# Kernel tuning notes

Hardware: AMD Instinct MI355X
Metric: run time of the kernel (lower is better)

The kernel has to match this reference:

```python
import jax, jax.numpy as jnp
import numpy as np

N_NODES = 100_000
E_OFF = 1_000_000
HID = 32
GF = 8
NF = 8
N_LAYERS = 3


def _mlp(h, W1, b1, W2, b2):
    # Linear -> ReLU -> Linear (matches MLP([in, hidden, out]))
    return jax.nn.relu(h @ W1 + b1) @ W2 + b2


def _seg_mean(v, idx, n):
    s = jax.ops.segment_sum(v, idx, num_segments=n)
    c = jax.ops.segment_sum(jnp.ones((v.shape[0], 1), v.dtype), idx, num_segments=n)
    return s / jnp.maximum(c, 1.0)


def _graphnet(x, row, col, eattr2, g, p):
    # GraphNet with global block: edge MLP -> mean-aggregate to nodes -> node MLP -> global MLP
    eW1, eb1, eW2, eb2, nW1, nb1, nW2, nb2, gW1, gb1, gW2, gb2 = p
    n, e = x.shape[0], row.shape[0]
    gE = jnp.broadcast_to(g, (e, g.shape[1]))
    e_emb = _mlp(jnp.concatenate([gE, x[row], x[col], eattr2], axis=1), eW1, eb1, eW2, eb2)
    agg = _seg_mean(e_emb, row, n)
    gN = jnp.broadcast_to(g, (n, g.shape[1]))
    n_emb = _mlp(jnp.concatenate([gN, x, agg], axis=1), nW1, nb1, nW2, nb2)
    g_new = _mlp(jnp.concatenate([n_emb.mean(0, keepdims=True), e_emb.mean(0, keepdims=True), g], axis=1),
                 gW1, gb1, gW2, gb2)
    return e_emb, n_emb, g_new


def setup_inputs() -> dict:
    key = jax.random.key(0)
    ks = jax.random.split(key, 24)
    a = jax.random.randint(ks[0], (E_OFF,), 0, N_NODES)
    b = jax.random.randint(ks[1], (E_OFF,), 0, N_NODES)
    d = jnp.arange(N_NODES)
    l_ei = jnp.stack([jnp.concatenate([jnp.maximum(a, b), d]),
                      jnp.concatenate([jnp.minimum(a, b), d])])  # lower triangular + diag
    c = jax.random.randint(ks[2], (E_OFF,), 0, N_NODES)
    e = jax.random.randint(ks[3], (E_OFF,), 0, N_NODES)
    u_ei = jnp.stack([jnp.concatenate([jnp.minimum(c, e), d]),
                      jnp.concatenate([jnp.maximum(c, e), d])])  # upper triangular + diag
    E = E_OFF + N_NODES
    x = jax.random.normal(ks[4], (N_NODES, NF), dtype=jnp.float32)
    l_attr = jax.random.normal(ks[5], (E, 1), dtype=jnp.float32)
    u_attr = jax.random.normal(ks[6], (E, 1), dtype=jnp.float32)

    def w(k, shape):
        return (jax.random.normal(k, shape, dtype=jnp.float32) / np.sqrt(shape[-2])).astype(jnp.float32)

    e_in = GF + 2 * NF + 1 + 1  # 26 (edge attr padded to 2: skip col, zeros where absent)
    n_in = GF + 1 + NF          # 17
    g_in = NF + 1 + GF          # 17
    return {
        'x': x, 'l_edge_index': l_ei, 'u_edge_index': u_ei,
        'l_edge_attr': l_attr, 'u_edge_attr': u_attr,
        'eW1': w(ks[7], (2, N_LAYERS, e_in, HID)), 'eb1': 0.01 * jax.random.normal(ks[8], (2, N_LAYERS, HID)),
        'eW2': w(ks[9], (2, N_LAYERS, HID, 1)), 'eb2': 0.01 * jax.random.normal(ks[10], (2, N_LAYERS, 1)),
        'nW1': w(ks[11], (2, N_LAYERS, n_in, HID)), 'nb1': 0.01 * jax.random.normal(ks[12], (2, N_LAYERS, HID)),
        'nW2': w(ks[13], (2, N_LAYERS, HID, NF)), 'nb2': 0.01 * jax.random.normal(ks[14], (2, N_LAYERS, NF)),
        'gW1': w(ks[15], (2, N_LAYERS, g_in, HID)), 'gb1': 0.01 * jax.random.normal(ks[16], (2, N_LAYERS, HID)),
        'gW2': w(ks[17], (2, N_LAYERS, HID, GF)), 'gb2': 0.01 * jax.random.normal(ks[18], (2, N_LAYERS, GF)),
    }


def reference(x, l_edge_index, u_edge_index, l_edge_attr, u_edge_attr,
              eW1, eb1, eW2, eb2, nW1, nb1, nW2, nb2, gW1, gb1, gW2, gb2):
    params = (eW1, eb1, eW2, eb2, nW1, nb1, nW2, nb2, gW1, gb1, gW2, gb2)
    lr, lc = l_edge_index[0], l_edge_index[1]
    ur, uc = u_edge_index[0], u_edge_index[1]
    g = jnp.zeros((1, GF), x.dtype)
    l_e, u_e = l_edge_attr, u_edge_attr
    l_a = l_edge_attr  # skip-connection edge features (original matrix values)
    zl, zu = jnp.zeros_like(l_edge_attr), jnp.zeros_like(u_edge_attr)
    for i in range(N_LAYERS):
        p1 = tuple(w[0, i] for w in params)
        p2 = tuple(w[1, i] for w in params)
        l_in = jnp.concatenate([l_e, l_a if i != 0 else zl], axis=1)  # zeros col == no skip (block 0)
        l_e, l_n, g = _graphnet(x, lr, lc, l_in, g, p1)
        u_in = jnp.concatenate([u_e, zu], axis=1)  # l2 never has skip; padded zeros col
        u_e, u_n, g = _graphnet(l_n, ur, uc, u_in, g, p2)
        # NOTE: node embeddings are NOT carried across MP blocks in the original
    l_vals = jnp.where(lr == lc, jnp.exp(l_e[:, 0]), l_e[:, 0])
    u_vals = jnp.where(ur == uc, jnp.exp(u_e[:, 0]), u_e[:, 0])
    return jnp.concatenate([l_vals, u_vals])
```

## Files before the change

### kernel.cpp

```cpp
#include <hip/hip_runtime.h>


typedef unsigned int u32;

#define NB_SHIFT 9
#define NB_SIZE 512
#define RSTRIDE 1104

__device__ __forceinline__ float wave_sum(float v) {
#pragma unroll
    for (int off = 32; off > 0; off >>= 1) v += __shfl_down(v, off, 64);
    return v;
}


__global__ __launch_bounds__(256) void hist_kernel(
    const int* __restrict__ lr, const int* __restrict__ ur,
    u32* __restrict__ hist, int E, int B) {
    __shared__ u32 h[256];
    const int t = threadIdx.x;
    if (t < B) h[t] = 0;
    __syncthreads();
    const int s = blockIdx.y;
    const int* rows = s ? ur : lr;
    for (int i = blockIdx.x * 256 + t; i < E; i += gridDim.x * 256)
        atomicAdd(&h[rows[i] >> NB_SHIFT], 1u);
    __syncthreads();
    if (t < B && h[t]) atomicAdd(&hist[s * B + t], h[t]);
}

__global__ __launch_bounds__(256) void scan_kernel(
    const u32* __restrict__ hist, u32* __restrict__ offs,
    u32* __restrict__ cur, int B) {
    __shared__ u32 sh[256];
    const int t = threadIdx.x;
    for (int s = 0; s < 2; ++s) {
        const u32 v = (t < B) ? hist[s * B + t] : 0u;
        sh[t] = v;
        __syncthreads();
#pragma unroll
        for (int off = 1; off < 256; off <<= 1) {
            const u32 add = (t >= off) ? sh[t - off] : 0u;
            __syncthreads();
            sh[t] += add;
            __syncthreads();
        }
        const u32 exc = sh[t] - v;
        if (t < B) {
            offs[s * (B + 1) + t] = exc;
            cur[s * B + t] = exc;
        }
        if (t == 255) offs[s * (B + 1) + B] = sh[255];
        __syncthreads();
    }
}

#define SCHUNK 4096
__global__ __launch_bounds__(256) void scatter_kernel(
    const int* __restrict__ lr, const int* __restrict__ ur,
    u32* __restrict__ cur, u32* __restrict__ list, int E, int B) {
    __shared__ u32 lcnt[256], lbase[256];
    const int t = threadIdx.x;
    const int s = blockIdx.y;
    const int* rows = s ? ur : lr;
    u32* mylist = list + (size_t)s * E;
    if (t < B) lcnt[t] = 0;
    __syncthreads();
    const int base_e = blockIdx.x * SCHUNK;
#pragma unroll
    for (int k = 0; k < SCHUNK / 256; ++k) {
        const int e = base_e + k * 256 + t;
        if (e < E) atomicAdd(&lcnt[rows[e] >> NB_SHIFT], 1u);
    }
    __syncthreads();
    if (t < B) {
        const u32 c = lcnt[t];
        lbase[t] = c ? atomicAdd(&cur[s * B + t], c) : 0u;
        lcnt[t] = 0;
    }
    __syncthreads();
#pragma unroll
    for (int k = 0; k < SCHUNK / 256; ++k) {
        const int e = base_e + k * 256 + t;
        if (e < E) {
            const int b = rows[e] >> NB_SHIFT;
            const u32 pos = lbase[b] + atomicAdd(&lcnt[b], 1u);
            mylist[pos] = (u32)e;
        }
    }
}


template <bool SKIP, bool GAGG, bool VALS, bool STORE, bool GCOMP>
__global__ __launch_bounds__(256) void edge_kernel(
    const float4* __restrict__ xf,
    const int* __restrict__ rows, const int* __restrict__ cols,
    const float* __restrict__ eprev,
    const float* __restrict__ skipattr,
    const float* __restrict__ W1,
    const float* __restrict__ b1,
    const float* __restrict__ W2,
    const float* __restrict__ b2,
    const float* __restrict__ gprev,
    float* __restrict__ gout,
    const float* __restrict__ pebins,
    const float* __restrict__ pnbins,
    const float* __restrict__ gW1, const float* __restrict__ gb1,
    const float* __restrict__ gW2, const float* __restrict__ gb2,
    float* __restrict__ ebins,
    float* __restrict__ e_out,
    float* __restrict__ vals_out,
    int E, int N, float inv_E) {
    __shared__ float gsh[8];
    __shared__ float biasE[32];
    __shared__ float wpart[4];
    const int t = threadIdx.x;
    if constexpr (GCOMP) {
        if (t < 64) {
            float nb[8];
#pragma unroll
            for (int q = 0; q < 8; ++q) nb[q] = pnbins[t * 16 + q];
            const float eb = pebins[t];
            float gin[17];
#pragma unroll
            for (int q = 0; q < 8; ++q) {
                const float s = wave_sum(nb[q]);
                gin[q] = __shfl(s, 0, 64) / (float)N;
            }
            const float es = wave_sum(eb);
            gin[8] = __shfl(es, 0, 64) * inv_E;
#pragma unroll
            for (int k = 0; k < 8; ++k) gin[9 + k] = gprev[k];
            float hv = 0.0f;
            if (t < 32) {
                hv = gb1[t];
#pragma unroll
                for (int k = 0; k < 17; ++k)
                    hv = fmaf(gin[k], gW1[k * 32 + t], hv);
                hv = fmaxf(hv, 0.0f);
            }
#pragma unroll
            for (int q = 0; q < 8; ++q) {
                const float c = (t < 32) ? hv * gW2[t * 8 + q] : 0.0f;
                const float s = wave_sum(c);
                if (t == 0) {
                    const float gv = gb2[q] + s;
                    gsh[q] = gv;
                    if (blockIdx.x == 0) gout[q] = gv;
                }
            }
        }
    } else {
        if (t < 8) gsh[t] = gprev[t];
    }
    __syncthreads();
    if (t < 32) {
        float v = b1[t];
#pragma unroll
        for (int k = 0; k < 8; ++k) v = fmaf(gsh[k], W1[k * 32 + t], v);
        biasE[t] = v;
    }
    __syncthreads();

    const int e = blockIdx.x * 256 + t;
    const bool valid = e < E;
    const int idx = valid ? e : 0;
    const int r = rows[idx];
    const int c = cols[idx];
    const float4 xr0 = xf[2 * r], xr1 = xf[2 * r + 1];
    const float4 xc0 = xf[2 * c], xc1 = xf[2 * c + 1];
    float in[18] = {xr0.x, xr0.y, xr0.z, xr0.w, xr1.x, xr1.y, xr1.z, xr1.w,
                    xc0.x, xc0.y, xc0.z, xc0.w, xc1.x, xc1.y, xc1.z, xc1.w,
                    eprev[idx], 0.0f};
    if constexpr (SKIP) in[17] = skipattr[idx];
    float h[32];
#pragma unroll
    for (int j = 0; j < 8; ++j) {
        const float4 b = reinterpret_cast<const float4*>(biasE)[j];
        h[4 * j + 0] = b.x; h[4 * j + 1] = b.y;
        h[4 * j + 2] = b.z; h[4 * j + 3] = b.w;
    }
    const float* __restrict__ Wk = W1 + 8 * 32;
#pragma unroll
    for (int k = 0; k < 18; ++k) {
        const float v = in[k];
#pragma unroll
        for (int j = 0; j < 32; ++j) h[j] = fmaf(v, Wk[k * 32 + j], h[j]);
    }
    float out = b2[0];
#pragma unroll
    for (int j = 0; j < 32; ++j) out = fmaf(fmaxf(h[j], 0.0f), W2[j], out);

    if (valid) {
        if constexpr (STORE) e_out[e] = out;
        if constexpr (VALS) vals_out[e] = (r == c) ? expf(out) : out;
    }
    if constexpr (GAGG) {
        const float s = wave_sum(valid ? out : 0.0f);
        if ((t & 63) == 0) wpart[t >> 6] = s;
        __syncthreads();
        if (t == 0)
            atomicAdd(&ebins[blockIdx.x & 63],
                      wpart[0] + wpart[1] + wpart[2] + wpart[3]);
    }
}


template <bool COUNT, bool STORE_N>
__global__ __launch_bounds__(1024) void aggnode_kernel(
    const u32* __restrict__ list, const u32* __restrict__ offs,
    const int* __restrict__ rows, const float* __restrict__ e_emb,
    const float4* __restrict__ xf,
    float* __restrict__ cntf,
    const float* __restrict__ g,
    const float* __restrict__ nW1, const float* __restrict__ nb1,
    const float* __restrict__ nW2, const float* __restrict__ nb2,
    float* __restrict__ n_out,
    float* __restrict__ nbins,
    int N) {
    __shared__ float sbin[NB_SIZE];
    __shared__ float cbin[NB_SIZE];
    __shared__ float biasN[32];
    __shared__ float npart[8][8];
    const int t = threadIdx.x;
    if (t < NB_SIZE) {
        sbin[t] = 0.0f;
        if constexpr (COUNT) cbin[t] = 0.0f;
    }
    if (t >= NB_SIZE && t < NB_SIZE + 32) {
        const int j = t - NB_SIZE;
        float v = nb1[j];
#pragma unroll
        for (int k = 0; k < 8; ++k) v = fmaf(g[k], nW1[k * 32 + j], v);
        biasN[j] = v;
    }
    __syncthreads();
    const int b = blockIdx.x;
    const u32 beg = offs[b], end = offs[b + 1];
    for (u32 i = beg + t; i < end; i += 1024) {
        const u32 eid = list[i];
        const float v = e_emb[eid];
        const int r = rows[eid];
        atomicAdd(&sbin[r & (NB_SIZE - 1)], v);
        if constexpr (COUNT) atomicAdd(&cbin[r & (NB_SIZE - 1)], 1.0f);
    }
    __syncthreads();

    const int n0 = b << NB_SHIFT;
    float o[8];
    const bool active = (t < NB_SIZE) && (n0 + t < N);
    if (t < NB_SIZE) {
        const int n = n0 + t;
        const int idx = active ? n : (N - 1);
        float cntv;
        if constexpr (COUNT) {
            cntv = cbin[t];
            if (active) cntf[n] = cntv;
        } else {
            cntv = cntf[idx];
        }
        const float agg = sbin[t] / fmaxf(cntv, 1.0f);
        const float4 x0 = xf[2 * idx], x1 = xf[2 * idx + 1];
        float in[9] = {x0.x, x0.y, x0.z, x0.w, x1.x, x1.y, x1.z, x1.w, agg};
        float h[32];
#pragma unroll
        for (int j = 0; j < 8; ++j) {
            const float4 bb = reinterpret_cast<const float4*>(biasN)[j];
            h[4 * j + 0] = bb.x; h[4 * j + 1] = bb.y;
            h[4 * j + 2] = bb.z; h[4 * j + 3] = bb.w;
        }
        const float* __restrict__ Wk = nW1 + 8 * 32;
#pragma unroll
        for (int k = 0; k < 9; ++k) {
            const float v = in[k];
#pragma unroll
            for (int j = 0; j < 32; ++j) h[j] = fmaf(v, Wk[k * 32 + j], h[j]);
        }
#pragma unroll
        for (int q = 0; q < 8; ++q) o[q] = nb2[q];
#pragma unroll
        for (int j = 0; j < 32; ++j) {
            const float hv = fmaxf(h[j], 0.0f);
#pragma unroll
            for (int q = 0; q < 8; ++q) o[q] = fmaf(hv, nW2[j * 8 + q], o[q]);
        }
        if constexpr (STORE_N) {
            if (active) {
                reinterpret_cast<float4*>(n_out)[2 * n] =
                    make_float4(o[0], o[1], o[2], o[3]);
                reinterpret_cast<float4*>(n_out)[2 * n + 1] =
                    make_float4(o[4], o[5], o[6], o[7]);
            }
        }
#pragma unroll
        for (int q = 0; q < 8; ++q) {
            const float s = wave_sum(active ? o[q] : 0.0f);
            if ((t & 63) == 0) npart[t >> 6][q] = s;
        }
    }
    __syncthreads();
    if (t < 8) {
        float a = 0.0f;
#pragma unroll
        for (int w = 0; w < 8; ++w) a += npart[w][t];
        atomicAdd(&nbins[(b & 63) * 16 + t], a);
    }
}

extern "C" void kernel_launch(void* const* d_in, const int* in_sizes, int n_in,
                              void* d_out, int out_size, void* d_ws,
                              size_t ws_size, hipStream_t stream) {
    const float* x = (const float*)d_in[0];
    const int* l_ei = (const int*)d_in[1];
    const int* u_ei = (const int*)d_in[2];
    const float* l_attr = (const float*)d_in[3];
    const float* u_attr = (const float*)d_in[4];
    const float* eW1 = (const float*)d_in[5];
    const float* eb1 = (const float*)d_in[6];
    const float* eW2 = (const float*)d_in[7];
    const float* eb2 = (const float*)d_in[8];
    const float* nW1 = (const float*)d_in[9];
    const float* nb1 = (const float*)d_in[10];
    const float* nW2 = (const float*)d_in[11];
    const float* nb2 = (const float*)d_in[12];
    const float* gW1 = (const float*)d_in[13];
    const float* gb1 = (const float*)d_in[14];
    const float* gW2 = (const float*)d_in[15];
    const float* gb2 = (const float*)d_in[16];

    const int E = in_sizes[3];
    const int N = in_sizes[0] / 8;
    const int B = (N + NB_SIZE - 1) >> NB_SHIFT;

    float* ws = (float*)d_ws;
    float* l_e = ws;
    float* u_e = l_e + E;
    float* l_n = u_e + E;
    float* cnt_l = l_n + (size_t)8 * N;
    float* cnt_u = cnt_l + N;
    float* gslot = cnt_u + N;
    u32* hist = (u32*)(gslot + 56);
    float* dyn_all = (float*)(hist + 2 * B);
    u32* offs = (u32*)(dyn_all + 5 * RSTRIDE);
    u32* cur = offs + 2 * (B + 1);
    u32* list = cur + 2 * B;

    const int* lr = l_ei;
    const int* lc = l_ei + E;
    const int* ur = u_ei;
    const int* uc = u_ei + E;
    const int eg = (E + 255) / 256;
    const int sg = (E + SCHUNK - 1) / SCHUNK;
    const float invE = 1.0f / (float)E;
    float* outL = (float*)d_out;
    float* outU = outL + E;
    const u32* offs_l = offs;
    const u32* offs_u = offs + (B + 1);
    const u32* list_l = list;
    const u32* list_u = list + E;

    hipMemsetAsync(gslot, 0, (size_t)(56 + 2 * B + 5 * RSTRIDE) * sizeof(float),
                   stream);
    hist_kernel<<<dim3(128, 2), 256, 0, stream>>>(lr, ur, hist, E, B);
    scan_kernel<<<1, 256, 0, stream>>>(hist, offs, cur, B);
    scatter_kernel<<<dim3(sg, 2), 256, 0, stream>>>(lr, ur, cur, list, E, B);

    const size_t wsl[6] = {0, 3, 1, 4, 2, 5};

    for (int j = 0; j < 6; ++j) {
        const bool lower = !(j & 1);
        const size_t sl = wsl[j];
        float* ebins = dyn_all + (size_t)(j <= 4 ? j : 4) * RSTRIDE;
        float* nbins = ebins + 64;
        const float* pe = (j >= 1) ? dyn_all + (size_t)(j - 1) * RSTRIDE : nullptr;
        const float* pn = (j >= 1) ? pe + 64 : nullptr;
        const size_t psl = (j >= 1) ? wsl[j - 1] : 0;
        const float4* exf = (const float4*)(lower ? x : l_n);
        const int* rows = lower ? lr : ur;
        const int* cols = lower ? lc : uc;
        const float* eprev = (j == 0) ? l_attr
                             : (j == 1) ? u_attr
                             : (lower ? l_e : u_e);
        float* e_out = lower ? l_e : u_e;
        const float* gprev = gslot + (size_t)(j >= 1 ? j - 1 : 0) * 8;
        float* gout = gslot + (size_t)j * 8;

#define EDGE_ARGS                                                             \
    exf, rows, cols, eprev, l_attr, eW1 + sl * 832, eb1 + sl * 32,            \
        eW2 + sl * 32, eb2 + sl, gprev, gout, pe, pn, gW1 + psl * 544,        \
        gb1 + psl * 32, gW2 + psl * 256, gb2 + psl * 8, ebins,                \
        e_out, (j == 4) ? outL : outU, E, N, invE

        switch (j) {
            case 0: edge_kernel<false, true, false, true, false>
                        <<<eg, 256, 0, stream>>>(EDGE_ARGS); break;
            case 1: edge_kernel<false, true, false, true, true>
                        <<<eg, 256, 0, stream>>>(EDGE_ARGS); break;
            case 2: edge_kernel<true, true, false, true, true>
                        <<<eg, 256, 0, stream>>>(EDGE_ARGS); break;
            case 3: edge_kernel<false, true, false, true, true>
                        <<<eg, 256, 0, stream>>>(EDGE_ARGS); break;
            case 4: edge_kernel<true, true, true, true, true>
                        <<<eg, 256, 0, stream>>>(EDGE_ARGS); break;
            case 5: edge_kernel<false, false, true, false, true>
                        <<<eg, 256, 0, stream>>>(EDGE_ARGS); break;
        }
#undef EDGE_ARGS

        if (j == 5) break;

        const u32* alist = lower ? list_l : list_u;
        const u32* aoffs = lower ? offs_l : offs_u;
        float* cntf = lower ? cnt_l : cnt_u;
        const float4* nxf = (const float4*)(lower ? x : l_n);

#define AGG_ARGS                                                              \
    alist, aoffs, rows, e_out, nxf, cntf, gslot + (size_t)j * 8,              \
        nW1 + sl * 544, nb1 + sl * 32, nW2 + sl * 256, nb2 + sl * 8, l_n,     \
        nbins, N

        switch (j) {
            case 0: aggnode_kernel<true, true>
                        <<<B, 1024, 0, stream>>>(AGG_ARGS); break;
            case 1: aggnode_kernel<true, false>
                        <<<B, 1024, 0, stream>>>(AGG_ARGS); break;
            case 2: aggnode_kernel<false, true>
                        <<<B, 1024, 0, stream>>>(AGG_ARGS); break;
            case 3: aggnode_kernel<false, false>
                        <<<B, 1024, 0, stream>>>(AGG_ARGS); break;
            case 4: aggnode_kernel<false, true>
                        <<<B, 1024, 0, stream>>>(AGG_ARGS); break;
        }
#undef AGG_ARGS
    }
}
```

Measured before the change: 548.2 us.

## Precompute per-node first-layer projections to replace per-edge gathers of node features

```diff
diff --git a/kernel.cpp b/kernel.cpp
--- a/kernel.cpp
+++ b/kernel.cpp
@@ -91,9 +91,40 @@
 }
 
 
+__global__ __launch_bounds__(256) void nodew_kernel(
+    const float4* __restrict__ xf, const float* __restrict__ W1,
+    float4* __restrict__ Atab, float4* __restrict__ Btab, int N) {
+    const int n = blockIdx.x * 256 + threadIdx.x;
+    if (n >= N) return;
+    const float4 x0 = xf[2 * n], x1 = xf[2 * n + 1];
+    const float xs[8] = {x0.x, x0.y, x0.z, x0.w, x1.x, x1.y, x1.z, x1.w};
+    float a[32], b[32];
+#pragma unroll
+    for (int j = 0; j < 32; ++j) { a[j] = 0.0f; b[j] = 0.0f; }
+    const float* __restrict__ WA = W1 + 8 * 32;
+    const float* __restrict__ WB = W1 + 16 * 32;
+#pragma unroll
+    for (int k = 0; k < 8; ++k) {
+        const float v = xs[k];
+#pragma unroll
+        for (int j = 0; j < 32; ++j) {
+            a[j] = fmaf(v, WA[k * 32 + j], a[j]);
+            b[j] = fmaf(v, WB[k * 32 + j], b[j]);
+        }
+    }
+    float4* An = Atab + 8 * (size_t)n;
+    float4* Bn = Btab + 8 * (size_t)n;
+#pragma unroll
+    for (int q = 0; q < 8; ++q) {
+        An[q] = make_float4(a[4 * q], a[4 * q + 1], a[4 * q + 2], a[4 * q + 3]);
+        Bn[q] = make_float4(b[4 * q], b[4 * q + 1], b[4 * q + 2], b[4 * q + 3]);
+    }
+}
+
+
 template <bool SKIP, bool GAGG, bool VALS, bool STORE, bool GCOMP>
 __global__ __launch_bounds__(256) void edge_kernel(
-    const float4* __restrict__ xf,
+    const float4* __restrict__ Atab, const float4* __restrict__ Btab,
     const int* __restrict__ rows, const int* __restrict__ cols,
     const float* __restrict__ eprev,
     const float* __restrict__ skipattr,
@@ -167,25 +198,29 @@
     const int idx = valid ? e : 0;
     const int r = rows[idx];
     const int c = cols[idx];
-    const float4 xr0 = xf[2 * r], xr1 = xf[2 * r + 1];
-    const float4 xc0 = xf[2 * c], xc1 = xf[2 * c + 1];
-    float in[18] = {xr0.x, xr0.y, xr0.z, xr0.w, xr1.x, xr1.y, xr1.z, xr1.w,
-                    xc0.x, xc0.y, xc0.z, xc0.w, xc1.x, xc1.y, xc1.z, xc1.w,
-                    eprev[idx], 0.0f};
-    if constexpr (SKIP) in[17] = skipattr[idx];
+    const float ep = eprev[idx];
+    float sk = 0.0f;
+    if constexpr (SKIP) sk = skipattr[idx];
+    const float4* __restrict__ Ar = Atab + 8 * (size_t)r;
+    const float4* __restrict__ Bc = Btab + 8 * (size_t)c;
+    const float* __restrict__ W24 = W1 + 24 * 32;
+    const float* __restrict__ W25 = W1 + 25 * 32;
     float h[32];
 #pragma unroll
-    for (int j = 0; j < 8; ++j) {
-        const float4 b = reinterpret_cast<const float4*>(biasE)[j];
-        h[4 * j + 0] = b.x; h[4 * j + 1] = b.y;
-        h[4 * j + 2] = b.z; h[4 * j + 3] = b.w;
-    }
-    const float* __restrict__ Wk = W1 + 8 * 32;
-#pragma unroll
-    for (int k = 0; k < 18; ++k) {
-        const float v = in[k];
-#pragma unroll
-        for (int j = 0; j < 32; ++j) h[j] = fmaf(v, Wk[k * 32 + j], h[j]);
+    for (int q = 0; q < 8; ++q) {
+        const float4 av = Ar[q];
+        const float4 bv = Bc[q];
+        const float4 bi = reinterpret_cast<const float4*>(biasE)[q];
+        h[4 * q + 0] = bi.x + av.x + bv.x;
+        h[4 * q + 1] = bi.y + av.y + bv.y;
+        h[4 * q + 2] = bi.z + av.z + bv.z;
+        h[4 * q + 3] = bi.w + av.w + bv.w;
+    }
+#pragma unroll
+    for (int j = 0; j < 32; ++j) h[j] = fmaf(ep, W24[j], h[j]);
+    if constexpr (SKIP) {
+#pragma unroll
+        for (int j = 0; j < 32; ++j) h[j] = fmaf(sk, W25[j], h[j]);
     }
     float out = b2[0];
 #pragma unroll
@@ -333,7 +368,9 @@
     const int B = (N + NB_SIZE - 1) >> NB_SHIFT;
 
     float* ws = (float*)d_ws;
-    float* l_e = ws;
+    float* Atab = ws;
+    float* Btab = Atab + (size_t)32 * N;
+    float* l_e = Btab + (size_t)32 * N;
     float* u_e = l_e + E;
     float* l_n = u_e + E;
     float* cnt_l = l_n + (size_t)8 * N;
@@ -350,6 +387,7 @@
     const int* ur = u_ei;
     const int* uc = u_ei + E;
     const int eg = (E + 255) / 256;
+    const int ng = (N + 255) / 256;
     const int sg = (E + SCHUNK - 1) / SCHUNK;
     const float invE = 1.0f / (float)E;
     float* outL = (float*)d_out;
@@ -375,7 +413,6 @@
         const float* pe = (j >= 1) ? dyn_all + (size_t)(j - 1) * RSTRIDE : nullptr;
         const float* pn = (j >= 1) ? pe + 64 : nullptr;
         const size_t psl = (j >= 1) ? wsl[j - 1] : 0;
-        const float4* exf = (const float4*)(lower ? x : l_n);
         const int* rows = lower ? lr : ur;
         const int* cols = lower ? lc : uc;
         const float* eprev = (j == 0) ? l_attr
@@ -385,11 +422,15 @@
         const float* gprev = gslot + (size_t)(j >= 1 ? j - 1 : 0) * 8;
         float* gout = gslot + (size_t)j * 8;
 
+        nodew_kernel<<<ng, 256, 0, stream>>>(
+            (const float4*)(lower ? x : l_n), eW1 + sl * 832,
+            (float4*)Atab, (float4*)Btab, N);
+
 #define EDGE_ARGS                                                             \
-    exf, rows, cols, eprev, l_attr, eW1 + sl * 832, eb1 + sl * 32,            \
-        eW2 + sl * 32, eb2 + sl, gprev, gout, pe, pn, gW1 + psl * 544,        \
-        gb1 + psl * 32, gW2 + psl * 256, gb2 + psl * 8, ebins,                \
-        e_out, (j == 4) ? outL : outU, E, N, invE
+    (const float4*)Atab, (const float4*)Btab, rows, cols, eprev, l_attr,      \
+        eW1 + sl * 832, eb1 + sl * 32, eW2 + sl * 32, eb2 + sl, gprev, gout,  \
+        pe, pn, gW1 + psl * 544, gb1 + psl * 32, gW2 + psl * 256,             \
+        gb2 + psl * 8, ebins, e_out, (j == 4) ? outL : outU, E, N, invE
 
         switch (j) {
             case 0: edge_kernel<false, true, false, true, false>
```

Result: slower. 741.0 us (+35.2%).
